# Kernel tuning notes

Measured on AMD Instinct MI355X. Metric: run time of the kernel, lower is better.

## Reference

```python
import jax, jax.numpy as jnp
import numpy as np

A, B, M, H, NMOL = 100000, 200000, 50000, 128, 4000
DEPTH = 5
MAX_NB = 8


def setup_inputs() -> dict:
    key = jax.random.key(0)
    ks = jax.random.split(key, 10)
    fatoms = jax.random.normal(ks[0], (A, 35), dtype=jnp.float32)
    fbonds = jax.random.normal(ks[1], (B, 40), dtype=jnp.float32)
    # index 0 of the combined message table is the zero padding message
    tree_message = jax.random.normal(ks[2], (M, H), dtype=jnp.float32).at[0].set(0.0)
    agraph = jax.random.randint(ks[3], (A, MAX_NB), 0, M + B, dtype=jnp.int32)
    bgraph = jax.random.randint(ks[4], (B, MAX_NB), 0, M + B, dtype=jnp.int32)
    mol_id = jnp.sort(jax.random.randint(ks[5], (A,), 0, NMOL, dtype=jnp.int32))
    W_i = jax.random.normal(ks[6], (40, H), dtype=jnp.float32) * 0.05
    W_h = jax.random.normal(ks[7], (H, H), dtype=jnp.float32) * 0.05
    W_o = jax.random.normal(ks[8], (35 + H, H), dtype=jnp.float32) * 0.05
    b_o = jax.random.normal(ks[9], (H,), dtype=jnp.float32) * 0.05
    return {"fatoms": fatoms, "fbonds": fbonds, "tree_message": tree_message,
            "agraph": agraph, "bgraph": bgraph, "mol_id": mol_id,
            "W_i": W_i, "W_h": W_h, "W_o": W_o, "b_o": b_o, "n_mols": NMOL}


def reference(fatoms, fbonds, tree_message, agraph, bgraph, mol_id, W_i, W_h, W_o, b_o, n_mols):
    binput = fbonds @ W_i                      # [B, H]
    graph_message = jax.nn.relu(binput)        # [B, H]
    for _ in range(DEPTH - 1):
        message = jnp.concatenate([tree_message, graph_message], axis=0)  # [M+B, H]
        nei = jnp.take(message, bgraph, axis=0).sum(axis=1)               # [B, H]
        graph_message = jax.nn.relu(binput + nei @ W_h)
    message = jnp.concatenate([tree_message, graph_message], axis=0)
    nei_a = jnp.take(message, agraph, axis=0).sum(axis=1)                 # [A, H]
    ainput = jnp.concatenate([fatoms, nei_a], axis=1)                     # [A, 35+H]
    atom_hiddens = jax.nn.relu(ainput @ W_o + b_o)                        # [A, H]
    sums = jax.ops.segment_sum(atom_hiddens, mol_id, num_segments=n_mols)
    counts = jax.ops.segment_sum(jnp.ones((atom_hiddens.shape[0],), dtype=atom_hiddens.dtype),
                                 mol_id, num_segments=n_mols)
    mol_vecs = sums / jnp.maximum(counts, 1.0)[:, None]                   # [n_mols, H]
    return mol_vecs
```

## Files before the change

kernel.cpp:

```cpp
#include <hip/hip_runtime.h>
#include <hip/hip_bf16.h>

#define AN 100000
#define BN 200000
#define MN 50000
#define HD 128
#define NMOL 4000
#define MAXNB 8
#define BSZ 24576

typedef unsigned short u16;
typedef unsigned int   u32;
typedef float f32x4 __attribute__((ext_vector_type(4)));
typedef short s16x8 __attribute__((ext_vector_type(8)));

__device__ __forceinline__ u16 f2bf(float x) {
    u32 u = __float_as_uint(x);
    return (u16)((u + 0x7fffu + ((u >> 16) & 1u)) >> 16);
}

__global__ __launch_bounds__(256) void k_prep(const float* __restrict__ tree,
                                              u16* __restrict__ tree_bf,
                                              const float* __restrict__ W_h,
                                              const float* __restrict__ W_i,
                                              const float* __restrict__ W_o,
                                              const float* __restrict__ b_o,
                                              u16* __restrict__ Bit,
                                              u16* __restrict__ Bat,
                                              const int* __restrict__ mol_id,
                                              float* __restrict__ counts,
                                              const float* __restrict__ fbonds,
                                              u16* __restrict__ fbp) {
    int blk = blockIdx.x, tid = threadIdx.x;
    if (blk < 6250) {
        int i = blk * 256 + tid;
        const float4 v = ((const float4*)tree)[i];
        uint2 r;
        r.x = (u32)f2bf(v.x) | ((u32)f2bf(v.y) << 16);
        r.y = (u32)f2bf(v.z) | ((u32)f2bf(v.w) << 16);
        ((uint2*)tree_bf)[i] = r;
    } else if (blk < 6442) {
        int i = (blk - 6250) * 256 + tid;
        int which = (i >= BSZ);
        int e = which ? i - BSZ : i;
        int j = e & 7, lane = (e >> 3) & 63, nt = (e >> 9) & 7, kt = e >> 12;
        int k = kt * 32 + (lane >> 4) * 8 + j;
        int n = nt * 16 + (lane & 15);
        if (!which) {
            float v = (k < 128) ? W_h[k * 128 + n] : ((k < 168) ? W_i[(k - 128) * 128 + n] : 0.f);
            Bit[e] = f2bf(v);
        } else {
            float v = (k < 128) ? W_o[(35 + k) * 128 + n]
                    : (k < 163) ? W_o[(k - 128) * 128 + n]
                    : (k == 163) ? b_o[n] : 0.f;
            Bat[e] = f2bf(v);
        }
    } else if (blk < 6458) {
        int m = (blk - 6442) * 256 + tid;
        if (m < NMOL) {
            int lo = 0, hi = AN;
            while (lo < hi) { int mid = (lo + hi) >> 1; if (mol_id[mid] < m) lo = mid + 1; else hi = mid; }
            int s = lo; lo = 0; hi = AN;
            while (lo < hi) { int mid = (lo + hi) >> 1; if (mol_id[mid] < m + 1) lo = mid + 1; else hi = mid; }
            counts[m] = (float)(lo - s);
        }
    } else {
        int q = (blk - 6458) * 256 + tid;
        if (q < 2000000) {
            const float4 v = ((const float4*)fbonds)[q];
            uint2 r;
            r.x = (u32)f2bf(v.x) | ((u32)f2bf(v.y) << 16);
            r.y = (u32)f2bf(v.z) | ((u32)f2bf(v.w) << 16);
            ((uint2*)fbp)[q] = r;
        }
    }
}

#define LDB 136
template <bool PK>
__global__ __launch_bounds__(256) void k_binput_mfma(const float* __restrict__ fbonds,
                                                     const u16* __restrict__ fbp,
                                                     const u16* __restrict__ Bsw,
                                                     u16* __restrict__ g0) {
    __shared__ __align__(16) u16 sA[64][LDB];
    int tid = threadIdx.x;
    int b0  = blockIdx.x * 64;
    if (PK) {
        const uint4* f4 = (const uint4*)fbp;
        for (int i = tid; i < 512; i += 256) {
            if (i < 320) {
                int row = i / 5, seg = i % 5;
                *(uint4*)&sA[row][seg * 8] = f4[(size_t)(b0 + row) * 5 + seg];
            } else {
                int j = i - 320, row = j / 3, seg = j % 3;
                *(uint4*)&sA[row][40 + seg * 8] = (uint4){0u, 0u, 0u, 0u};
            }
        }
    } else {
        for (int i = tid; i < 64 * 64; i += 256) {
            int b = i >> 6, c = i & 63;
            float v = (c < 40) ? fbonds[(size_t)(b0 + b) * 40 + c] : 0.f;
            sA[b][c] = f2bf(v);
        }
    }
    __syncthreads();
    int lane = tid & 63, wv = tid >> 6;
    int am = lane & 15, aq = lane >> 4;
    s16x8 afr[2];
#pragma unroll
    for (int kt = 0; kt < 2; ++kt)
        afr[kt] = *(const s16x8*)&sA[wv * 16 + am][kt * 32 + aq * 8];
    f32x4 acc[8];
#pragma unroll
    for (int nt = 0; nt < 8; ++nt) acc[nt] = (f32x4){0.f, 0.f, 0.f, 0.f};
    const s16x8* B8 = (const s16x8*)Bsw;
#pragma unroll
    for (int kt = 0; kt < 2; ++kt)
#pragma unroll
        for (int nt = 0; nt < 8; ++nt) {
            s16x8 bfr = B8[((4 + kt) * 8 + nt) * 64 + lane];
            acc[nt] = __builtin_amdgcn_mfma_f32_16x16x32_bf16(afr[kt], bfr, acc[nt], 0, 0, 0);
        }
#pragma unroll
    for (int nt = 0; nt < 8; ++nt)
#pragma unroll
        for (int r = 0; r < 4; ++r)
            sA[wv * 16 + aq * 4 + r][nt * 16 + am] = f2bf(fmaxf(acc[nt][r], 0.f));
    __syncthreads();
#pragma unroll
    for (int s = 0; s < 4; ++s) {
        int e = tid + s * 256;
        int row = e >> 4, seg = e & 15;
        *(uint4*)&g0[((size_t)b0 + row) * HD + seg * 8] = *(const uint4*)&sA[row][seg * 8];
    }
}

#define LDA 200

__device__ __forceinline__ void gather16(u16 (*sA)[LDA], const int (*sidx)[MAXNB],
                                         const u16* __restrict__ tree_bf,
                                         const u16* __restrict__ tin, int tid) {
    int l = tid & 15, tb = tid >> 4;
#pragma unroll
    for (int pp = 0; pp < 2; ++pp) {
        int r0 = tb + (2 * pp) * 16;
        int r1 = tb + (2 * pp + 1) * 16;
        uint4 v[2][8];
#pragma unroll
        for (int j = 0; j < 8; ++j) {
            int idx = sidx[r0][j];
            const u16* base = (idx < MN) ? tree_bf + (size_t)idx * HD
                                         : tin + (size_t)(idx - MN) * HD;
            v[0][j] = ((const uint4*)base)[l];
        }
#pragma unroll
        for (int j = 0; j < 8; ++j) {
            int idx = sidx[r1][j];
            const u16* base = (idx < MN) ? tree_bf + (size_t)idx * HD
                                         : tin + (size_t)(idx - MN) * HD;
            v[1][j] = ((const uint4*)base)[l];
        }
#pragma unroll
        for (int h = 0; h < 2; ++h) {
            float a[8] = {0.f, 0.f, 0.f, 0.f, 0.f, 0.f, 0.f, 0.f};
#pragma unroll
            for (int j = 0; j < 8; ++j) {
                a[0] += __uint_as_float(v[h][j].x << 16);
                a[1] += __uint_as_float(v[h][j].x & 0xffff0000u);
                a[2] += __uint_as_float(v[h][j].y << 16);
                a[3] += __uint_as_float(v[h][j].y & 0xffff0000u);
                a[4] += __uint_as_float(v[h][j].z << 16);
                a[5] += __uint_as_float(v[h][j].z & 0xffff0000u);
                a[6] += __uint_as_float(v[h][j].w << 16);
                a[7] += __uint_as_float(v[h][j].w & 0xffff0000u);
            }
            uint4 r;
            r.x = (u32)f2bf(a[0]) | ((u32)f2bf(a[1]) << 16);
            r.y = (u32)f2bf(a[2]) | ((u32)f2bf(a[3]) << 16);
            r.z = (u32)f2bf(a[4]) | ((u32)f2bf(a[5]) << 16);
            r.w = (u32)f2bf(a[6]) | ((u32)f2bf(a[7]) << 16);
            *(uint4*)&sA[h == 0 ? r0 : r1][l * 8] = r;
        }
    }
}

template <bool PK>
__global__ __launch_bounds__(256) void k_iter_mfma(const u16* __restrict__ tree_bf,
                                                   const u16* __restrict__ tin,
                                                   const float* __restrict__ fbonds,
                                                   const u16* __restrict__ fbp,
                                                   const int* __restrict__ bgraph,
                                                   const u16* __restrict__ Bsw,
                                                   u16* __restrict__ tout) {
    __shared__ __align__(16) u16 sA[64][LDA];
    __shared__ int sidx[64][MAXNB];
    int tid = threadIdx.x;
    int b0  = blockIdx.x * 64;

    for (int i = tid; i < 64 * MAXNB; i += 256)
        sidx[i >> 3][i & 7] = bgraph[(size_t)(b0 + (i >> 3)) * MAXNB + (i & 7)];
    if (PK) {
        const uint4* f4 = (const uint4*)fbp;
        for (int i = tid; i < 512; i += 256) {
            if (i < 320) {
                int row = i / 5, seg = i % 5;
                *(uint4*)&sA[row][128 + seg * 8] = f4[(size_t)(b0 + row) * 5 + seg];
            } else {
                int j = i - 320, row = j / 3, seg = j % 3;
                *(uint4*)&sA[row][168 + seg * 8] = (uint4){0u, 0u, 0u, 0u};
            }
        }
    } else {
        for (int i = tid; i < 64 * 64; i += 256) {
            int b = i >> 6, c = i & 63;
            float v = (c < 40) ? fbonds[(size_t)(b0 + b) * 40 + c] : 0.f;
            sA[b][128 + c] = f2bf(v);
        }
    }
    __syncthreads();

    gather16(sA, sidx, tree_bf, tin, tid);
    __syncthreads();

    int lane = tid & 63, wv = tid >> 6;
    int am = lane & 15, aq = lane >> 4;
    s16x8 afr[6];
#pragma unroll
    for (int kt = 0; kt < 6; ++kt)
        afr[kt] = *(const s16x8*)&sA[wv * 16 + am][kt * 32 + aq * 8];
    f32x4 acc[8];
#pragma unroll
    for (int nt = 0; nt < 8; ++nt) acc[nt] = (f32x4){0.f, 0.f, 0.f, 0.f};
    const s16x8* B8 = (const s16x8*)Bsw;
#pragma unroll
    for (int kt = 0; kt < 6; ++kt)
#pragma unroll
        for (int nt = 0; nt < 8; ++nt) {
            s16x8 bfr = B8[(kt * 8 + nt) * 64 + lane];
            acc[nt] = __builtin_amdgcn_mfma_f32_16x16x32_bf16(afr[kt], bfr, acc[nt], 0, 0, 0);
        }
#pragma unroll
    for (int nt = 0; nt < 8; ++nt)
#pragma unroll
        for (int r = 0; r < 4; ++r)
            sA[wv * 16 + aq * 4 + r][nt * 16 + am] = f2bf(fmaxf(acc[nt][r], 0.f));
    __syncthreads();
#pragma unroll
    for (int s = 0; s < 4; ++s) {
        int e = tid + s * 256;
        int row = e >> 4, seg = e & 15;
        *(uint4*)&tout[((size_t)b0 + row) * HD + seg * 8] = *(const uint4*)&sA[row][seg * 8];
    }
}

__global__ __launch_bounds__(256) void k_atom_mfma(const u16* __restrict__ tree_bf,
                                                   const u16* __restrict__ gfin,
                                                   const float* __restrict__ fatoms,
                                                   const int* __restrict__ agraph,
                                                   const int* __restrict__ mol_id,
                                                   const u16* __restrict__ Bsw,
                                                   float* __restrict__ sums) {
    __shared__ __align__(16) char smem[64 * 132 * sizeof(float)];
    u16   (*sA)[LDA] = (u16 (*)[LDA])smem;
    float* sC        = (float*)smem;
    __shared__ int sidx[64][MAXNB];
    __shared__ int smol[64];
    int tid = threadIdx.x;
    int a0  = blockIdx.x * 64;

    for (int i = tid; i < 64 * MAXNB; i += 256) {
        int a = a0 + (i >> 3);
        sidx[i >> 3][i & 7] = (a < AN) ? agraph[(size_t)a * MAXNB + (i & 7)] : 0;
    }
    if (tid < 64) smol[tid] = (a0 + tid < AN) ? mol_id[a0 + tid] : -1;
    for (int i = tid; i < 64 * 64; i += 256) {
        int b = i >> 6, c = i & 63;
        float v = 0.f;
        if (a0 + b < AN) {
            if (c < 35) v = fatoms[(size_t)(a0 + b) * 35 + c];
            else if (c == 35) v = 1.f;
        }
        sA[b][128 + c] = f2bf(v);
    }
    __syncthreads();
    gather16(sA, sidx, tree_bf, gfin, tid);
    __syncthreads();

    int lane = tid & 63, wv = tid >> 6;
    int am = lane & 15, aq = lane >> 4;
    s16x8 afr[6];
#pragma unroll
    for (int kt = 0; kt < 6; ++kt)
        afr[kt] = *(const s16x8*)&sA[wv * 16 + am][kt * 32 + aq * 8];
    __syncthreads();

    f32x4 acc[8];
#pragma unroll
    for (int nt = 0; nt < 8; ++nt) acc[nt] = (f32x4){0.f, 0.f, 0.f, 0.f};
    const s16x8* B8 = (const s16x8*)Bsw;
#pragma unroll
    for (int kt = 0; kt < 6; ++kt)
#pragma unroll
        for (int nt = 0; nt < 8; ++nt) {
            s16x8 bfr = B8[(kt * 8 + nt) * 64 + lane];
            acc[nt] = __builtin_amdgcn_mfma_f32_16x16x32_bf16(afr[kt], bfr, acc[nt], 0, 0, 0);
        }
#pragma unroll
    for (int nt = 0; nt < 8; ++nt)
#pragma unroll
        for (int r = 0; r < 4; ++r) {
            int row = wv * 16 + aq * 4 + r;
            int col = nt * 16 + am;
            sC[row * 132 + col] = fmaxf(acc[nt][r], 0.f);
        }
    __syncthreads();

    {
        int c = tid & 127, half = tid >> 7;
        int base = half * 32;
        float run = 0.f;
        int cur = smol[base];
        for (int r = 0; r < 32; ++r) {
            int row = base + r;
            int mv = smol[row];
            if (mv != cur) {
                if (cur >= 0) atomicAdd(&sums[(size_t)cur * HD + c], run);
                run = 0.f; cur = mv;
            }
            run += sC[row * 132 + c];
        }
        if (cur >= 0) atomicAdd(&sums[(size_t)cur * HD + c], run);
    }
}

__global__ __launch_bounds__(256) void k_div(const float* __restrict__ sums,
                                             const float* __restrict__ counts,
                                             float* __restrict__ out) {
    int i = blockIdx.x * 256 + threadIdx.x;
    if (i < NMOL * HD) out[i] = sums[i] / fmaxf(counts[i >> 7], 1.f);
}

extern "C" void kernel_launch(void* const* d_in, const int* in_sizes, int n_in,
                              void* d_out, int out_size, void* d_ws, size_t ws_size,
                              hipStream_t stream) {
    const float* fatoms = (const float*)d_in[0];
    const float* fbonds = (const float*)d_in[1];
    const float* tree   = (const float*)d_in[2];
    const int*   agraph = (const int*)d_in[3];
    const int*   bgraph = (const int*)d_in[4];
    const int*   mol_id = (const int*)d_in[5];
    const float* W_i    = (const float*)d_in[6];
    const float* W_h    = (const float*)d_in[7];
    const float* W_o    = (const float*)d_in[8];
    const float* b_o    = (const float*)d_in[9];
    float* out = (float*)d_out;

    size_t tbl   = (size_t)BN * HD;
    size_t treeN = (size_t)MN * HD;
    size_t fbN   = (size_t)BN * 40;
    size_t redN  = (size_t)(NMOL * HD + NMOL);

    size_t need_base = (2 * tbl + treeN + 2 * BSZ) * 2 + redN * 4;
    size_t need_pack = need_base + fbN * 2;

    if (ws_size < need_base) {
        hipMemsetAsync(d_out, 0, (size_t)out_size * sizeof(float), stream);
        return;
    }
    bool pk = (ws_size >= need_pack);

    u16* t0      = (u16*)d_ws;
    u16* t1      = t0 + tbl;
    u16* tree_bf = t1 + tbl;
    u16* Bit     = tree_bf + treeN;
    u16* Bat     = Bit + BSZ;
    u16* fbp     = pk ? (Bat + BSZ) : nullptr;
    float* sums   = (float*)(pk ? (fbp + fbN) : (Bat + BSZ));
    float* counts = sums + (size_t)NMOL * HD;

    hipMemsetAsync(sums, 0, (size_t)NMOL * HD * sizeof(float), stream);
    k_prep<<<pk ? 14271 : 6458, 256, 0, stream>>>(tree, tree_bf, W_h, W_i, W_o, b_o,
                                                  Bit, Bat, mol_id, counts, fbonds, fbp);
    if (pk)
        k_binput_mfma<true><<<BN / 64, 256, 0, stream>>>(fbonds, fbp, Bit, t0);
    else
        k_binput_mfma<false><<<BN / 64, 256, 0, stream>>>(fbonds, fbp, Bit, t0);

    u16* cur = t0;
    u16* nxt = t1;
    for (int it = 0; it < 4; ++it) {
        if (pk)
            k_iter_mfma<true><<<BN / 64, 256, 0, stream>>>(tree_bf, cur, fbonds, fbp,
                                                           bgraph, Bit, nxt);
        else
            k_iter_mfma<false><<<BN / 64, 256, 0, stream>>>(tree_bf, cur, fbonds, fbp,
                                                            bgraph, Bit, nxt);
        u16* t = cur; cur = nxt; nxt = t;
    }
    k_atom_mfma<<<(AN + 63) / 64, 256, 0, stream>>>(tree_bf, cur, fatoms, agraph,
                                                    mol_id, Bat, sums);
    k_div<<<(NMOL * HD) / 256, 256, 0, stream>>>(sums, counts, out);
}
```

Measured before the change: 484.0 us.

## Fold sums memset and binput GEMM into the prep kernel

```diff
diff --git a/kernel.cpp b/kernel.cpp
--- a/kernel.cpp
+++ b/kernel.cpp
@@ -29,8 +29,12 @@
                                               u16* __restrict__ Bat,
                                               const int* __restrict__ mol_id,
                                               float* __restrict__ counts,
+                                              float* __restrict__ sums,
                                               const float* __restrict__ fbonds,
-                                              u16* __restrict__ fbp) {
+                                              u16* __restrict__ fbp,
+                                              u16* __restrict__ g0) {
+    __shared__ __align__(16) u16 sA[64][136];
+    __shared__ __align__(16) u16 sW[8192];
     int blk = blockIdx.x, tid = threadIdx.x;
     if (blk < 6250) {
         int i = blk * 256 + tid;
@@ -64,8 +68,53 @@
             while (lo < hi) { int mid = (lo + hi) >> 1; if (mol_id[mid] < m + 1) lo = mid + 1; else hi = mid; }
             counts[m] = (float)(lo - s);
         }
+    } else if (blk < 6958) {
+        int i = (blk - 6458) * 256 + tid;
+        if (i < NMOL * HD / 4) ((float4*)sums)[i] = (float4){0.f, 0.f, 0.f, 0.f};
+    } else if (blk < 10083) {
+        int b0 = (blk - 6958) * 64;
+        for (int e = tid; e < 8192; e += 256) {
+            int j = e & 7, lane = (e >> 3) & 63, nt = (e >> 9) & 7, kt = e >> 12;
+            int k = kt * 32 + (lane >> 4) * 8 + j;
+            int n = nt * 16 + (lane & 15);
+            sW[e] = f2bf((k < 40) ? W_i[k * 128 + n] : 0.f);
+        }
+        for (int i = tid; i < 64 * 64; i += 256) {
+            int b = i >> 6, c = i & 63;
+            float v = (c < 40) ? fbonds[(size_t)(b0 + b) * 40 + c] : 0.f;
+            sA[b][c] = f2bf(v);
+        }
+        __syncthreads();
+        int lane = tid & 63, wv = tid >> 6;
+        int am = lane & 15, aq = lane >> 4;
+        s16x8 afr[2];
+#pragma unroll
+        for (int kt = 0; kt < 2; ++kt)
+            afr[kt] = *(const s16x8*)&sA[wv * 16 + am][kt * 32 + aq * 8];
+        f32x4 acc[8];
+#pragma unroll
+        for (int nt = 0; nt < 8; ++nt) acc[nt] = (f32x4){0.f, 0.f, 0.f, 0.f};
+#pragma unroll
+        for (int kt = 0; kt < 2; ++kt)
+#pragma unroll
+            for (int nt = 0; nt < 8; ++nt) {
+                s16x8 bfr = *(const s16x8*)&sW[((kt * 8 + nt) * 64 + lane) * 8];
+                acc[nt] = __builtin_amdgcn_mfma_f32_16x16x32_bf16(afr[kt], bfr, acc[nt], 0, 0, 0);
+            }
+#pragma unroll
+        for (int nt = 0; nt < 8; ++nt)
+#pragma unroll
+            for (int r = 0; r < 4; ++r)
+                sA[wv * 16 + aq * 4 + r][nt * 16 + am] = f2bf(fmaxf(acc[nt][r], 0.f));
+        __syncthreads();
+#pragma unroll
+        for (int s = 0; s < 4; ++s) {
+            int e = tid + s * 256;
+            int row = e >> 4, seg = e & 15;
+            *(uint4*)&g0[((size_t)b0 + row) * HD + seg * 8] = *(const uint4*)&sA[row][seg * 8];
+        }
     } else {
-        int q = (blk - 6458) * 256 + tid;
+        int q = (blk - 10083) * 256 + tid;
         if (q < 2000000) {
             const float4 v = ((const float4*)fbonds)[q];
             uint2 r;
@@ -73,65 +122,6 @@
             r.y = (u32)f2bf(v.z) | ((u32)f2bf(v.w) << 16);
             ((uint2*)fbp)[q] = r;
         }
-    }
-}
-
-#define LDB 136
-template <bool PK>
-__global__ __launch_bounds__(256) void k_binput_mfma(const float* __restrict__ fbonds,
-                                                     const u16* __restrict__ fbp,
-                                                     const u16* __restrict__ Bsw,
-                                                     u16* __restrict__ g0) {
-    __shared__ __align__(16) u16 sA[64][LDB];
-    int tid = threadIdx.x;
-    int b0  = blockIdx.x * 64;
-    if (PK) {
-        const uint4* f4 = (const uint4*)fbp;
-        for (int i = tid; i < 512; i += 256) {
-            if (i < 320) {
-                int row = i / 5, seg = i % 5;
-                *(uint4*)&sA[row][seg * 8] = f4[(size_t)(b0 + row) * 5 + seg];
-            } else {
-                int j = i - 320, row = j / 3, seg = j % 3;
-                *(uint4*)&sA[row][40 + seg * 8] = (uint4){0u, 0u, 0u, 0u};
-            }
-        }
-    } else {
-        for (int i = tid; i < 64 * 64; i += 256) {
-            int b = i >> 6, c = i & 63;
-            float v = (c < 40) ? fbonds[(size_t)(b0 + b) * 40 + c] : 0.f;
-            sA[b][c] = f2bf(v);
-        }
-    }
-    __syncthreads();
-    int lane = tid & 63, wv = tid >> 6;
-    int am = lane & 15, aq = lane >> 4;
-    s16x8 afr[2];
-#pragma unroll
-    for (int kt = 0; kt < 2; ++kt)
-        afr[kt] = *(const s16x8*)&sA[wv * 16 + am][kt * 32 + aq * 8];
-    f32x4 acc[8];
-#pragma unroll
-    for (int nt = 0; nt < 8; ++nt) acc[nt] = (f32x4){0.f, 0.f, 0.f, 0.f};
-    const s16x8* B8 = (const s16x8*)Bsw;
-#pragma unroll
-    for (int kt = 0; kt < 2; ++kt)
-#pragma unroll
-        for (int nt = 0; nt < 8; ++nt) {
-            s16x8 bfr = B8[((4 + kt) * 8 + nt) * 64 + lane];
-            acc[nt] = __builtin_amdgcn_mfma_f32_16x16x32_bf16(afr[kt], bfr, acc[nt], 0, 0, 0);
-        }
-#pragma unroll
-    for (int nt = 0; nt < 8; ++nt)
-#pragma unroll
-        for (int r = 0; r < 4; ++r)
-            sA[wv * 16 + aq * 4 + r][nt * 16 + am] = f2bf(fmaxf(acc[nt][r], 0.f));
-    __syncthreads();
-#pragma unroll
-    for (int s = 0; s < 4; ++s) {
-        int e = tid + s * 256;
-        int row = e >> 4, seg = e & 15;
-        *(uint4*)&g0[((size_t)b0 + row) * HD + seg * 8] = *(const uint4*)&sA[row][seg * 8];
     }
 }
 
@@ -378,13 +368,9 @@
     float* sums   = (float*)(pk ? (fbp + fbN) : (Bat + BSZ));
     float* counts = sums + (size_t)NMOL * HD;
 
-    hipMemsetAsync(sums, 0, (size_t)NMOL * HD * sizeof(float), stream);
-    k_prep<<<pk ? 14271 : 6458, 256, 0, stream>>>(tree, tree_bf, W_h, W_i, W_o, b_o,
-                                                  Bit, Bat, mol_id, counts, fbonds, fbp);
-    if (pk)
-        k_binput_mfma<true><<<BN / 64, 256, 0, stream>>>(fbonds, fbp, Bit, t0);
-    else
-        k_binput_mfma<false><<<BN / 64, 256, 0, stream>>>(fbonds, fbp, Bit, t0);
+    k_prep<<<pk ? 17896 : 10083, 256, 0, stream>>>(tree, tree_bf, W_h, W_i, W_o, b_o,
+                                                   Bit, Bat, mol_id, counts, sums,
+                                                   fbonds, fbp, t0);
 
     u16* cur = t0;
     u16* nxt = t1;
```

After: 521.2 us. +7.7%, slower.
